# Kernel optimization log

Measured on AMD Instinct MI355X. Metric: run time of the kernel, lower is better.

Reference implementation:

```python
import jax, jax.numpy as jnp
import numpy as np

MAX_VAL = 255.0
C1 = (0.01 * MAX_VAL) ** 2
C2 = (0.03 * MAX_VAL) ** 2


def _gauss_window(ws, sigma, channel=3):
    x = np.arange(ws, dtype=np.float64)
    g = np.exp(-((x - ws // 2) ** 2) / (2.0 * sigma ** 2))
    g = g / g.sum()
    w2 = np.outer(g, g).astype(np.float32)  # [ws, ws]
    w = np.broadcast_to(w2, (channel, 1, ws, ws)).copy()  # depthwise OIHW
    return jnp.asarray(w)


def _dwconv(x, w, pad):
    # depthwise conv2d, NCHW, groups == channels
    return jax.lax.conv_general_dilated(
        x, w, window_strides=(1, 1), padding=[(pad, pad), (pad, pad)],
        dimension_numbers=("NCHW", "OIHW", "NCHW"),
        feature_group_count=x.shape[1])


def _ssim_pair(img1, img2):
    _, c, h, w = img1.shape
    ws = min(h, w, 11)
    sigma = 1.5 * ws / 11.0
    win = _gauss_window(ws, sigma, c)
    pad = ws // 2
    mu1 = _dwconv(img1, win, pad)
    mu2 = _dwconv(img2, win, pad)
    mu1_sq, mu2_sq, mu1_mu2 = mu1 * mu1, mu2 * mu2, mu1 * mu2
    sigma1_sq = _dwconv(img1 * img1, win, pad) - mu1_sq
    sigma2_sq = _dwconv(img2 * img2, win, pad) - mu2_sq
    sigma12 = _dwconv(img1 * img2, win, pad) - mu1_mu2
    V1 = 2.0 * sigma12 + C2
    V2 = sigma1_sq + sigma2_sq + C2
    ssim_map = (2.0 * mu1_mu2 + C1) * V1 / ((mu1_sq + mu2_sq + C1) * V2)
    mcs_map = V1 / V2
    return ssim_map.mean(), mcs_map.mean()


def _avg_pool2(x):
    B, C, H, W = x.shape
    return x.reshape(B, C, H // 2, 2, W // 2, 2).mean(axis=(3, 5))


def _ms_ssim(img1, img2, levels=5):
    weight = jnp.array([0.0448, 0.2856, 0.3001, 0.2363, 0.1333], jnp.float32)
    msssim, mcs = [], []
    for _ in range(levels):
        s, m = _ssim_pair(img1, img2)
        msssim.append(s)
        mcs.append(m)
        img1 = _avg_pool2(img1)
        img2 = _avg_pool2(img2)
    msssim = jnp.stack(msssim)
    mcs = jnp.stack(mcs)
    value = jnp.prod(mcs[: levels - 1] ** weight[: levels - 1]) * msssim[levels - 1] ** weight[levels - 1]
    return 1.0 - value


def _l1_oss(img1, img2):
    _, c, h, w = img1.shape
    ws = min(h, w, 7)
    sigma = 1.1 * ws / 7.0
    win = _gauss_window(ws, sigma, c)
    return _dwconv(jnp.abs(img1 - img2), win, ws // 2).mean()


def _clr_loss(img1, img3):
    _, c, h, w = img1.shape
    ws = min(h, w, 29)
    sigma = ws / 6.0
    win = _gauss_window(ws, sigma, c)
    pad = ws // 2
    mu1 = _dwconv(img1, win, pad)
    mu3 = _dwconv(img3, win, pad)
    cw = [-0.000519, 0.07633, -0.173433, 1.435936, -1.894404, 1.556091]
    # Horner evaluation of cw[5]*x^5 + ... + cw[1]*x + cw[0]
    mu1 = ((((cw[5] * mu1 + cw[4]) * mu1 + cw[3]) * mu1 + cw[2]) * mu1 + cw[1]) * mu1 + cw[0]
    wgray = jnp.array([0.299, 0.587, 0.144], jnp.float32).reshape(1, 3, 1, 1)
    mug1 = (mu1 * wgray).sum(axis=1, keepdims=True)  # 1x1 conv over channels
    mug3 = (mu3 * wgray).sum(axis=1, keepdims=True)
    me1 = mug1.mean(axis=(2, 3), keepdims=True)
    me3 = mug3.mean(axis=(2, 3), keepdims=True)
    sc = me1 / me3
    return jnp.abs(mu1 - mu3 * sc).mean()


def setup_inputs() -> dict:
    key = jax.random.key(0)
    k1, k2, k3 = jax.random.split(key, 3)
    shape = (16, 3, 512, 512)
    return {
        "img1": jax.random.uniform(k1, shape, dtype=jnp.float32),
        "img2": jax.random.uniform(k2, shape, dtype=jnp.float32),
        "img3": jax.random.uniform(k3, shape, dtype=jnp.float32),
    }


def reference(img1, img2, img3):
    l1v = _l1_oss(img1, img2)
    clrv = _clr_loss(img1, img3)
    ssimv = _ms_ssim(img1, img2)
    return 0.4 * ssimv + 0.4 * l1v + 0.2 * clrv
```

## Files before the change

### kernel.cpp

```cpp
#include <hip/hip_runtime.h>
#include <hip/hip_fp16.h>
#include <cmath>

typedef float f2 __attribute__((ext_vector_type(2)));

struct GW7  { float g[7];  };
struct GW11 { float g[11]; };
struct GW29 { float g[29]; };

static void make_gauss(int ws, double sigma, float* out) {
    double t[32]; double s = 0.0;
    int c = ws / 2;
    for (int i = 0; i < ws; ++i) { double d = i - c; t[i] = exp(-(d * d) / (2.0 * sigma * sigma)); s += t[i]; }
    for (int i = 0; i < ws; ++i) out[i] = (float)(t[i] / s);
}

#define ACC_SLOTS 44
#define ACC_BYTES (ACC_SLOTS * 64 * sizeof(double))

__device__ __forceinline__ float poly5(float x) {
    float r = fmaf(1.556091f, x, -1.894404f);
    r = fmaf(r, x, 1.435936f);
    r = fmaf(r, x, -0.173433f);
    r = fmaf(r, x, 0.07633f);
    r = fmaf(r, x, -0.000519f);
    return r;
}

__device__ __forceinline__ float border7(int p, const GW7& gw) {
    if (p >= 3 && p <= 508) return 1.f;
    float r = 0.f;
    #pragma unroll
    for (int k = 0; k < 7; ++k) { int q = p + 3 - k; if (q >= 0 && q < 512) r += gw.g[k]; }
    return r;
}

template<bool INTER>
__global__ __launch_bounds__(256) void ssim_kernel(
    const float* __restrict__ Aim, const float* __restrict__ Bim, const f2* __restrict__ AB,
    int H, int tpp, int tilesX, GW11 gw, GW7 g7, double* __restrict__ acc, int level,
    f2* __restrict__ pooled, int Ho)
{
    constexpr int TILE = 32, IN = 42, SP2 = 46, RP2 = 34;
    __shared__ f2 lds[2 * IN * RP2];
    __shared__ float red[12];
    f2* s    = lds;
    f2* r_mu = lds;
    f2* r_sq = lds + IN * RP2;

    const int tid = threadIdx.x;
    const int bid = blockIdx.x;
    const int plane = bid / tpp;
    const int t = bid - plane * tpp;
    const int ty = t / tilesX, tx = t - ty * tilesX;
    const size_t base = (size_t)plane * H * H;
    const int oy = ty * TILE - 5, ox = tx * TILE - 5;

    for (int i = tid; i < IN * IN; i += 256) {
        int y = i / IN, x = i - y * IN;
        int gy = oy + y, gx = ox + x;
        bool ok = (gy >= 0) && (gy < H) && (gx >= 0) && (gx < H);
        size_t o = base + (size_t)gy * H + gx;
        f2 v = {0.f, 0.f};
        if (ok) {
            if (INTER) v = AB[o];
            else { v.x = Aim[o]; v.y = Bim[o]; }
        }
        s[y * SP2 + x] = v;
    }
    __syncthreads();

    f2 v[18];
    const int ry = tid >> 2, rx0 = (tid & 3) * 8;
    if (tid < IN * 4) {
        #pragma unroll
        for (int l = 0; l < 18; ++l) v[l] = s[ry * SP2 + rx0 + l];
    }
    if (pooled) {
        int py = tid >> 4, px = tid & 15;
        int a = (5 + 2 * py) * SP2 + 5 + 2 * px;
        f2 u = s[a] + s[a + 1] + s[a + SP2] + s[a + SP2 + 1];
        pooled[(size_t)plane * Ho * Ho + (size_t)(ty * 16 + py) * Ho + (tx * 16 + px)] = 0.25f * u;
    }
    float l1p = 0.f;
    if (level == 0) {
        #pragma unroll
        for (int jj = 0; jj < 4; ++jj) {
            int p = jj * 256 + tid;
            int py = p >> 5, px = p & 31;
            f2 u = s[(5 + py) * SP2 + 5 + px];
            float w = border7(ty * 32 + py, g7) * border7(tx * 32 + px, g7);
            l1p += w * fabsf(u.x - u.y);
        }
    }
    __syncthreads();

    if (tid < IN * 4) {
        #pragma unroll
        for (int j = 0; j < 8; ++j) {
            f2 a = {0.f, 0.f};
            #pragma unroll
            for (int k = 0; k < 11; ++k) a = gw.g[k] * v[j + k] + a;
            r_mu[ry * RP2 + rx0 + j] = a;
        }
        #pragma unroll
        for (int l = 0; l < 18; ++l) {
            f2 w;
            w.x = fmaf(v[l].x, v[l].x, v[l].y * v[l].y);
            w.y = v[l].x * v[l].y;
            v[l] = w;
        }
        #pragma unroll
        for (int j = 0; j < 8; ++j) {
            f2 a = {0.f, 0.f};
            #pragma unroll
            for (int k = 0; k < 11; ++k) a = gw.g[k] * v[j + k] + a;
            r_sq[ry * RP2 + rx0 + j] = a;
        }
    }
    __syncthreads();

    const int y0 = (tid >> 5) * 4, x = tid & 31;
    float lss = 0.f, lmc = 0.f;
    {
        f2 mu[4], q[4];
        {
            f2 u[14];
            #pragma unroll
            for (int l = 0; l < 14; ++l) u[l] = r_mu[(y0 + l) * RP2 + x];
            #pragma unroll
            for (int j = 0; j < 4; ++j) {
                f2 a = {0.f, 0.f};
                #pragma unroll
                for (int k = 0; k < 11; ++k) a = gw.g[k] * u[j + k] + a;
                mu[j] = a;
            }
        }
        {
            f2 u[14];
            #pragma unroll
            for (int l = 0; l < 14; ++l) u[l] = r_sq[(y0 + l) * RP2 + x];
            #pragma unroll
            for (int j = 0; j < 4; ++j) {
                f2 a = {0.f, 0.f};
                #pragma unroll
                for (int k = 0; k < 11; ++k) a = gw.g[k] * u[j + k] + a;
                q[j] = a;
            }
        }
        #pragma unroll
        for (int j = 0; j < 4; ++j) {
            float m1 = mu[j].x, m2 = mu[j].y;
            float P = m1 * m2;
            float S = fmaf(m1, m1, m2 * m2);
            float V1 = 2.f * (q[j].y - P) + 58.5225f;
            float V2 = (q[j].x - S) + 58.5225f;
            float num = (2.f * P + 6.5025f) * V1;
            float SC = S + 6.5025f;
            float inv = __builtin_amdgcn_rcpf(SC * V2);
            lss = fmaf(num, inv, lss);
            lmc = fmaf(V1 * SC, inv, lmc);
        }
    }
    #pragma unroll
    for (int o = 32; o > 0; o >>= 1) {
        lss += __shfl_down(lss, o); lmc += __shfl_down(lmc, o); l1p += __shfl_down(l1p, o);
    }
    if ((tid & 63) == 0) {
        int g = tid >> 6;
        red[g * 3] = lss; red[g * 3 + 1] = lmc; red[g * 3 + 2] = l1p;
    }
    __syncthreads();
    if (tid == 0) {
        float a = red[0] + red[3] + red[6] + red[9];
        float m = red[1] + red[4] + red[7] + red[10];
        int stripe = bid & 63;
        atomicAdd(&acc[(0 + level) * 64 + stripe], (double)a);
        atomicAdd(&acc[(5 + level) * 64 + stripe], (double)m);
        if (level == 0) {
            float l1 = red[2] + red[5] + red[8] + red[11];
            atomicAdd(&acc[10 * 64 + stripe], (double)l1);
        }
    }
}

template<int MODE>
__global__ __launch_bounds__(256) void clr_conv(
    const float* __restrict__ img1, const float* __restrict__ img3,
    __half2* __restrict__ pbuf, GW29 gw, double* __restrict__ acc)
{
    constexpr int IN = 60, SP2 = 62, RP2 = 34;
    __shared__ f2 lds[IN * SP2];
    __shared__ float red[8];
    __shared__ float sc_sh;
    f2* s = lds;
    f2* r = lds;

    const int tid = threadIdx.x, bid = blockIdx.x;
    const int plane = bid >> 8, t = bid & 255;
    const int ty = t >> 4, tx = t & 15;
    const int b = plane / 3, c = plane - b * 3;
    const float wg = (c == 0) ? 0.299f : (c == 1 ? 0.587f : 0.144f);
    const size_t base = (size_t)plane * (512 * 512);
    const int oy = ty * 32 - 14, ox = tx * 32 - 14;

    if (MODE == 2 && tid < 64) {
        double m1 = acc[(12 + b) * 64 + tid];
        double m3 = acc[(28 + b) * 64 + tid];
        #pragma unroll
        for (int o = 32; o > 0; o >>= 1) { m1 += __shfl_down(m1, o); m3 += __shfl_down(m3, o); }
        if (tid == 0) sc_sh = (float)(m1 / m3);
    }

    for (int i = tid; i < IN * IN; i += 256) {
        int y = i / IN, x = i - y * IN;
        int gy = oy + y, gx = ox + x;
        bool ok = (gy >= 0) && (gy < 512) && (gx >= 0) && (gx < 512);
        size_t o = base + (size_t)gy * 512 + gx;
        f2 v = {0.f, 0.f};
        if (ok) { v.x = img1[o]; v.y = img3[o]; }
        s[y * SP2 + x] = v;
    }
    __syncthreads();

    f2 v[36];
    const int ry = tid >> 2, rx0 = (tid & 3) * 8;
    if (tid < IN * 4) {
        #pragma unroll
        for (int l = 0; l < 36; ++l) v[l] = s[ry * SP2 + rx0 + l];
    }
    __syncthreads();
    if (tid < IN * 4) {
        #pragma unroll
        for (int j = 0; j < 8; ++j) {
            f2 a = {0.f, 0.f};
            #pragma unroll
            for (int k = 0; k < 29; ++k) a = gw.g[k] * v[j + k] + a;
            r[ry * RP2 + rx0 + j] = a;
        }
    }
    __syncthreads();

    const int y0 = (tid >> 5) * 4, x = tid & 31;
    f2 mu[4];
    {
        f2 u[32];
        #pragma unroll
        for (int l = 0; l < 32; ++l) u[l] = r[(y0 + l) * RP2 + x];
        #pragma unroll
        for (int j = 0; j < 4; ++j) {
            f2 a = {0.f, 0.f};
            #pragma unroll
            for (int k = 0; k < 29; ++k) a = gw.g[k] * u[j + k] + a;
            mu[j] = a;
        }
    }
    float p1 = 0.f, p3 = 0.f;
    #pragma unroll
    for (int j = 0; j < 4; ++j) {
        float p = poly5(mu[j].x);
        if (MODE == 2) {
            p1 += fabsf(p - mu[j].y * sc_sh);
        } else {
            p1 += p; p3 += mu[j].y;
            if (MODE == 0)
                pbuf[base + (size_t)(ty * 32 + y0 + j) * 512 + (tx * 32 + x)] =
                    __floats2half2_rn(p, mu[j].y);
        }
    }
    if (MODE != 2) { p1 *= wg; p3 *= wg; }
    #pragma unroll
    for (int o = 32; o > 0; o >>= 1) { p1 += __shfl_down(p1, o); p3 += __shfl_down(p3, o); }
    if ((tid & 63) == 0) { red[(tid >> 6) * 2] = p1; red[(tid >> 6) * 2 + 1] = p3; }
    __syncthreads();
    if (tid == 0) {
        float a1 = red[0] + red[2] + red[4] + red[6];
        int stripe = bid & 63;
        if (MODE == 2) {
            atomicAdd(&acc[11 * 64 + stripe], (double)a1);
        } else {
            float a3 = red[1] + red[3] + red[5] + red[7];
            atomicAdd(&acc[(12 + b) * 64 + stripe], (double)a1);
            atomicAdd(&acc[(28 + b) * 64 + stripe], (double)a3);
        }
    }
}

__global__ __launch_bounds__(256) void clr_fin(
    const __half2* __restrict__ pbuf, double* __restrict__ acc)
{
    __shared__ float red[4];
    __shared__ float sc_sh;
    const int tid = threadIdx.x, bid = blockIdx.x;
    const int b = bid / 192, sub = bid - b * 192;
    if (tid < 64) {
        double m1 = acc[(12 + b) * 64 + tid];
        double m3 = acc[(28 + b) * 64 + tid];
        #pragma unroll
        for (int o = 32; o > 0; o >>= 1) { m1 += __shfl_down(m1, o); m3 += __shfl_down(m3, o); }
        if (tid == 0) sc_sh = (float)(m1 / m3);
    }
    __syncthreads();
    const float sc = sc_sh;
    const size_t bo = (size_t)b * 786432 + (size_t)sub * 4096;
    float s = 0.f;
    #pragma unroll
    for (int it = 0; it < 8; ++it) {
        size_t i = bo + it * 512 + tid * 2;
        float2 a = __half22float2(pbuf[i]);
        float2 c = __half22float2(pbuf[i + 1]);
        s += fabsf(a.x - a.y * sc) + fabsf(c.x - c.y * sc);
    }
    #pragma unroll
    for (int o = 32; o > 0; o >>= 1) s += __shfl_down(s, o);
    if ((tid & 63) == 0) red[tid >> 6] = s;
    __syncthreads();
    if (tid == 0)
        atomicAdd(&acc[11 * 64 + (bid & 63)], (double)(red[0] + red[1] + red[2] + red[3]));
}

__global__ void finalize_kernel(const double* __restrict__ acc, float* __restrict__ out)
{
    __shared__ double sums[ACC_SLOTS];
    int t = threadIdx.x;
    if (t < ACC_SLOTS) {
        double s = 0.0;
        for (int i = 0; i < 64; ++i) s += acc[t * 64 + i];
        sums[t] = s;
    }
    __syncthreads();
    if (t == 0) {
        const double w[5] = {0.0448, 0.2856, 0.3001, 0.2363, 0.1333};
        double value = 1.0;
        for (int l = 0; l < 5; ++l) {
            double dim = (double)(512 >> l);
            double cnt = 48.0 * dim * dim;
            double mval = (l < 4) ? (sums[5 + l] / cnt) : (sums[l] / cnt);
            value *= pow(mval, w[l]);
        }
        double n0 = 48.0 * 512.0 * 512.0;
        double l1v = sums[10] / n0;
        double clrv = sums[11] / n0;
        out[0] = (float)(0.4 * (1.0 - value) + 0.4 * l1v + 0.2 * clrv);
    }
}

extern "C" void kernel_launch(void* const* d_in, const int* in_sizes, int n_in,
                              void* d_out, int out_size, void* d_ws, size_t ws_size,
                              hipStream_t stream)
{
    (void)in_sizes; (void)n_in; (void)out_size;
    const float* img1 = (const float*)d_in[0];
    const float* img2 = (const float*)d_in[1];
    const float* img3 = (const float*)d_in[2];
    float* out = (float*)d_out;
    double* acc = (double*)d_ws;

    GW11 g11; make_gauss(11, 1.5, g11.g);
    GW7  g7;  make_gauss(7, 1.1, g7.g);
    GW29 g29; make_gauss(29, 29.0 / 6.0, g29.g);

    hipMemsetAsync(d_ws, 0, ACC_BYTES, stream);

    f2* pyr = (f2*)((char*)d_ws + 32768);
    size_t offs[4];
    offs[0] = 0;
    offs[1] = offs[0] + (size_t)48 * 256 * 256;
    offs[2] = offs[1] + (size_t)48 * 128 * 128;
    offs[3] = offs[2] + (size_t)48 * 64 * 64;
    const size_t PYRF2 = offs[3] + (size_t)48 * 32 * 32;

    const f2* cur = nullptr;
    int H = 512;
    for (int l = 0; l < 5; ++l) {
        int tilesX = H / 32; int tpp = tilesX * tilesX;
        f2* pooled = (l < 4) ? (pyr + offs[l]) : nullptr;
        int Ho = H / 2;
        if (l == 0)
            ssim_kernel<false><<<48 * tpp, 256, 0, stream>>>(
                img1, img2, nullptr, H, tpp, tilesX, g11, g7, acc, l, pooled, Ho);
        else
            ssim_kernel<true><<<48 * tpp, 256, 0, stream>>>(
                nullptr, nullptr, cur, H, tpp, tilesX, g11, g7, acc, l, pooled, Ho);
        cur = pooled; H = Ho;
    }

    const size_t poff = 32768 + PYRF2 * sizeof(f2);
    const size_t PBYTES = (size_t)48 * 512 * 512 * sizeof(__half2);
    __half2* pbuf = (__half2*)((char*)d_ws + poff);
    if (ws_size >= poff + PBYTES) {
        clr_conv<0><<<12288, 256, 0, stream>>>(img1, img3, pbuf, g29, acc);
        clr_fin<<<3072, 256, 0, stream>>>(pbuf, acc);
    } else {
        clr_conv<1><<<12288, 256, 0, stream>>>(img1, img3, pbuf, g29, acc);
        clr_conv<2><<<12288, 256, 0, stream>>>(img1, img3, pbuf, g29, acc);
    }

    finalize_kernel<<<1, 64, 0, stream>>>(acc, out);
}
```

Before: 236.3 us.

## Stream convolution taps to cut register pressure and split LDS buffers

The separable Gaussian passes in the SSIM and colour kernels now accumulate outputs while streaming input values, instead of holding whole input windows in registers. This lowers register use and may raise occupancy. The SSIM kernel gives the source tile and the two row-pass results their own LDS buffers with odd strides, which removes one barrier and aims to reduce bank conflicts but uses more shared memory. The colour kernel loads its 60-row halo in two 30-row chunks with 240 threads doing the horizontal pass, trading an extra barrier pair for a smaller staging buffer.

```diff
diff --git a/kernel.cpp b/kernel.cpp
--- a/kernel.cpp
+++ b/kernel.cpp
@@ -35,18 +35,19 @@
     return r;
 }
 
+#define SSP 47
+#define SRP 33
 template<bool INTER>
 __global__ __launch_bounds__(256) void ssim_kernel(
     const float* __restrict__ Aim, const float* __restrict__ Bim, const f2* __restrict__ AB,
     int H, int tpp, int tilesX, GW11 gw, GW7 g7, double* __restrict__ acc, int level,
     f2* __restrict__ pooled, int Ho)
 {
-    constexpr int TILE = 32, IN = 42, SP2 = 46, RP2 = 34;
-    __shared__ f2 lds[2 * IN * RP2];
+    constexpr int TILE = 32, IN = 42;
+    __shared__ f2 s[IN * SSP];
+    __shared__ f2 r_mu[IN * SRP];
+    __shared__ f2 r_sq[IN * SRP];
     __shared__ float red[12];
-    f2* s    = lds;
-    f2* r_mu = lds;
-    f2* r_sq = lds + IN * RP2;
 
     const int tid = threadIdx.x;
     const int bid = blockIdx.x;
@@ -66,20 +67,40 @@
             if (INTER) v = AB[o];
             else { v.x = Aim[o]; v.y = Bim[o]; }
         }
-        s[y * SP2 + x] = v;
-    }
-    __syncthreads();
-
-    f2 v[18];
-    const int ry = tid >> 2, rx0 = (tid & 3) * 8;
+        s[y * SSP + x] = v;
+    }
+    __syncthreads();
+
     if (tid < IN * 4) {
-        #pragma unroll
-        for (int l = 0; l < 18; ++l) v[l] = s[ry * SP2 + rx0 + l];
+        const int ry = tid >> 2, rx0 = (tid & 3) * 8;
+        f2 mu[8], q[8];
+        #pragma unroll
+        for (int j = 0; j < 8; ++j) { mu[j] = (f2){0.f, 0.f}; q[j] = (f2){0.f, 0.f}; }
+        #pragma unroll
+        for (int l = 0; l < 18; ++l) {
+            f2 val = s[ry * SSP + rx0 + l];
+            f2 sq;
+            sq.x = fmaf(val.x, val.x, val.y * val.y);
+            sq.y = val.x * val.y;
+            #pragma unroll
+            for (int j = 0; j < 8; ++j) {
+                if (l - j >= 0 && l - j < 11) {
+                    float g = gw.g[l - j];
+                    mu[j] = g * val + mu[j];
+                    q[j]  = g * sq  + q[j];
+                }
+            }
+        }
+        #pragma unroll
+        for (int j = 0; j < 8; ++j) {
+            r_mu[ry * SRP + rx0 + j] = mu[j];
+            r_sq[ry * SRP + rx0 + j] = q[j];
+        }
     }
     if (pooled) {
         int py = tid >> 4, px = tid & 15;
-        int a = (5 + 2 * py) * SP2 + 5 + 2 * px;
-        f2 u = s[a] + s[a + 1] + s[a + SP2] + s[a + SP2 + 1];
+        int a = (5 + 2 * py) * SSP + 5 + 2 * px;
+        f2 u = s[a] + s[a + 1] + s[a + SSP] + s[a + SSP + 1];
         pooled[(size_t)plane * Ho * Ho + (size_t)(ty * 16 + py) * Ho + (tx * 16 + px)] = 0.25f * u;
     }
     float l1p = 0.f;
@@ -88,34 +109,9 @@
         for (int jj = 0; jj < 4; ++jj) {
             int p = jj * 256 + tid;
             int py = p >> 5, px = p & 31;
-            f2 u = s[(5 + py) * SP2 + 5 + px];
+            f2 u = s[(5 + py) * SSP + 5 + px];
             float w = border7(ty * 32 + py, g7) * border7(tx * 32 + px, g7);
             l1p += w * fabsf(u.x - u.y);
-        }
-    }
-    __syncthreads();
-
-    if (tid < IN * 4) {
-        #pragma unroll
-        for (int j = 0; j < 8; ++j) {
-            f2 a = {0.f, 0.f};
-            #pragma unroll
-            for (int k = 0; k < 11; ++k) a = gw.g[k] * v[j + k] + a;
-            r_mu[ry * RP2 + rx0 + j] = a;
-        }
-        #pragma unroll
-        for (int l = 0; l < 18; ++l) {
-            f2 w;
-            w.x = fmaf(v[l].x, v[l].x, v[l].y * v[l].y);
-            w.y = v[l].x * v[l].y;
-            v[l] = w;
-        }
-        #pragma unroll
-        for (int j = 0; j < 8; ++j) {
-            f2 a = {0.f, 0.f};
-            #pragma unroll
-            for (int k = 0; k < 11; ++k) a = gw.g[k] * v[j + k] + a;
-            r_sq[ry * RP2 + rx0 + j] = a;
         }
     }
     __syncthreads();
@@ -124,29 +120,23 @@
     float lss = 0.f, lmc = 0.f;
     {
         f2 mu[4], q[4];
-        {
-            f2 u[14];
-            #pragma unroll
-            for (int l = 0; l < 14; ++l) u[l] = r_mu[(y0 + l) * RP2 + x];
-            #pragma unroll
-            for (int j = 0; j < 4; ++j) {
-                f2 a = {0.f, 0.f};
-                #pragma unroll
-                for (int k = 0; k < 11; ++k) a = gw.g[k] * u[j + k] + a;
-                mu[j] = a;
-            }
-        }
-        {
-            f2 u[14];
-            #pragma unroll
-            for (int l = 0; l < 14; ++l) u[l] = r_sq[(y0 + l) * RP2 + x];
-            #pragma unroll
-            for (int j = 0; j < 4; ++j) {
-                f2 a = {0.f, 0.f};
-                #pragma unroll
-                for (int k = 0; k < 11; ++k) a = gw.g[k] * u[j + k] + a;
-                q[j] = a;
-            }
+        #pragma unroll
+        for (int j = 0; j < 4; ++j) mu[j] = (f2){0.f, 0.f};
+        #pragma unroll
+        for (int l = 0; l < 14; ++l) {
+            f2 val = r_mu[(y0 + l) * SRP + x];
+            #pragma unroll
+            for (int j = 0; j < 4; ++j)
+                if (l - j >= 0 && l - j < 11) mu[j] = gw.g[l - j] * val + mu[j];
+        }
+        #pragma unroll
+        for (int j = 0; j < 4; ++j) q[j] = (f2){0.f, 0.f};
+        #pragma unroll
+        for (int l = 0; l < 14; ++l) {
+            f2 val = r_sq[(y0 + l) * SRP + x];
+            #pragma unroll
+            for (int j = 0; j < 4; ++j)
+                if (l - j >= 0 && l - j < 11) q[j] = gw.g[l - j] * val + q[j];
         }
         #pragma unroll
         for (int j = 0; j < 4; ++j) {
@@ -184,17 +174,17 @@
     }
 }
 
+#define CSP 63
+#define CRP 33
 template<int MODE>
 __global__ __launch_bounds__(256) void clr_conv(
     const float* __restrict__ img1, const float* __restrict__ img3,
     __half2* __restrict__ pbuf, GW29 gw, double* __restrict__ acc)
 {
-    constexpr int IN = 60, SP2 = 62, RP2 = 34;
-    __shared__ f2 lds[IN * SP2];
+    __shared__ f2 sc[30 * CSP];
+    __shared__ f2 r[60 * CRP];
     __shared__ float red[8];
     __shared__ float sc_sh;
-    f2* s = lds;
-    f2* r = lds;
 
     const int tid = threadIdx.x, bid = blockIdx.x;
     const int plane = bid >> 8, t = bid & 255;
@@ -212,48 +202,46 @@
         if (tid == 0) sc_sh = (float)(m1 / m3);
     }
 
-    for (int i = tid; i < IN * IN; i += 256) {
-        int y = i / IN, x = i - y * IN;
-        int gy = oy + y, gx = ox + x;
-        bool ok = (gy >= 0) && (gy < 512) && (gx >= 0) && (gx < 512);
-        size_t o = base + (size_t)gy * 512 + gx;
-        f2 v = {0.f, 0.f};
-        if (ok) { v.x = img1[o]; v.y = img3[o]; }
-        s[y * SP2 + x] = v;
-    }
-    __syncthreads();
-
-    f2 v[36];
-    const int ry = tid >> 2, rx0 = (tid & 3) * 8;
-    if (tid < IN * 4) {
-        #pragma unroll
-        for (int l = 0; l < 36; ++l) v[l] = s[ry * SP2 + rx0 + l];
-    }
-    __syncthreads();
-    if (tid < IN * 4) {
-        #pragma unroll
-        for (int j = 0; j < 8; ++j) {
-            f2 a = {0.f, 0.f};
-            #pragma unroll
-            for (int k = 0; k < 29; ++k) a = gw.g[k] * v[j + k] + a;
-            r[ry * RP2 + rx0 + j] = a;
-        }
-    }
-    __syncthreads();
+    #pragma unroll
+    for (int ck = 0; ck < 2; ++ck) {
+        for (int i = tid; i < 30 * 60; i += 256) {
+            int y = i / 60, x = i - y * 60;
+            int gy = oy + ck * 30 + y, gx = ox + x;
+            bool ok = (gy >= 0) && (gy < 512) && (gx >= 0) && (gx < 512);
+            size_t o = base + (size_t)gy * 512 + gx;
+            f2 v = {0.f, 0.f};
+            if (ok) { v.x = img1[o]; v.y = img3[o]; }
+            sc[y * CSP + x] = v;
+        }
+        __syncthreads();
+        if (tid < 240) {
+            int yl = tid >> 3, x0 = (tid & 7) * 4;
+            f2 a[4];
+            #pragma unroll
+            for (int j = 0; j < 4; ++j) a[j] = (f2){0.f, 0.f};
+            #pragma unroll
+            for (int l = 0; l < 32; ++l) {
+                f2 val = sc[yl * CSP + x0 + l];
+                #pragma unroll
+                for (int j = 0; j < 4; ++j)
+                    if (l - j >= 0 && l - j < 29) a[j] = gw.g[l - j] * val + a[j];
+            }
+            #pragma unroll
+            for (int j = 0; j < 4; ++j) r[(ck * 30 + yl) * CRP + x0 + j] = a[j];
+        }
+        __syncthreads();
+    }
 
     const int y0 = (tid >> 5) * 4, x = tid & 31;
     f2 mu[4];
-    {
-        f2 u[32];
-        #pragma unroll
-        for (int l = 0; l < 32; ++l) u[l] = r[(y0 + l) * RP2 + x];
-        #pragma unroll
-        for (int j = 0; j < 4; ++j) {
-            f2 a = {0.f, 0.f};
-            #pragma unroll
-            for (int k = 0; k < 29; ++k) a = gw.g[k] * u[j + k] + a;
-            mu[j] = a;
-        }
+    #pragma unroll
+    for (int j = 0; j < 4; ++j) mu[j] = (f2){0.f, 0.f};
+    #pragma unroll
+    for (int l = 0; l < 32; ++l) {
+        f2 val = r[(y0 + l) * CRP + x];
+        #pragma unroll
+        for (int j = 0; j < 4; ++j)
+            if (l - j >= 0 && l - j < 29) mu[j] = gw.g[l - j] * val + mu[j];
     }
     float p1 = 0.f, p3 = 0.f;
     #pragma unroll
```

Result: slower. 263.0 us (+11.3%).

## Load CLR conv rows directly from global with float4 and repad LDS strides

Applied to the files above, without the earlier changes.

The CLR Gaussian conv kernel no longer stages the 60x60 input tile in shared memory. Each thread reads its row segment from global memory with float4 loads into registers and runs the horizontal 29-tap pass there, processing img1 and img3 one after the other. This removes a staging pass and a barrier and shrinks LDS use. Separately, the LDS row strides in both kernels become odd (49 and 33 f2 elements) to reduce bank conflicts. The trade-offs are more register pressure and redundant global reads of the overlapping halo, which the cache has to absorb.

```diff
diff --git a/kernel.cpp b/kernel.cpp
--- a/kernel.cpp
+++ b/kernel.cpp
@@ -35,18 +35,20 @@
     return r;
 }
 
+#define SSP 49
+#define SRP 33
 template<bool INTER>
 __global__ __launch_bounds__(256) void ssim_kernel(
     const float* __restrict__ Aim, const float* __restrict__ Bim, const f2* __restrict__ AB,
     int H, int tpp, int tilesX, GW11 gw, GW7 g7, double* __restrict__ acc, int level,
     f2* __restrict__ pooled, int Ho)
 {
-    constexpr int TILE = 32, IN = 42, SP2 = 46, RP2 = 34;
-    __shared__ f2 lds[2 * IN * RP2];
+    constexpr int TILE = 32, IN = 42;
+    __shared__ f2 lds[2 * IN * SRP];
     __shared__ float red[12];
     f2* s    = lds;
     f2* r_mu = lds;
-    f2* r_sq = lds + IN * RP2;
+    f2* r_sq = lds + IN * SRP;
 
     const int tid = threadIdx.x;
     const int bid = blockIdx.x;
@@ -66,7 +68,7 @@
             if (INTER) v = AB[o];
             else { v.x = Aim[o]; v.y = Bim[o]; }
         }
-        s[y * SP2 + x] = v;
+        s[y * SSP + x] = v;
     }
     __syncthreads();
 
@@ -74,12 +76,12 @@
     const int ry = tid >> 2, rx0 = (tid & 3) * 8;
     if (tid < IN * 4) {
         #pragma unroll
-        for (int l = 0; l < 18; ++l) v[l] = s[ry * SP2 + rx0 + l];
+        for (int l = 0; l < 18; ++l) v[l] = s[ry * SSP + rx0 + l];
     }
     if (pooled) {
         int py = tid >> 4, px = tid & 15;
-        int a = (5 + 2 * py) * SP2 + 5 + 2 * px;
-        f2 u = s[a] + s[a + 1] + s[a + SP2] + s[a + SP2 + 1];
+        int a = (5 + 2 * py) * SSP + 5 + 2 * px;
+        f2 u = s[a] + s[a + 1] + s[a + SSP] + s[a + SSP + 1];
         pooled[(size_t)plane * Ho * Ho + (size_t)(ty * 16 + py) * Ho + (tx * 16 + px)] = 0.25f * u;
     }
     float l1p = 0.f;
@@ -88,7 +90,7 @@
         for (int jj = 0; jj < 4; ++jj) {
             int p = jj * 256 + tid;
             int py = p >> 5, px = p & 31;
-            f2 u = s[(5 + py) * SP2 + 5 + px];
+            f2 u = s[(5 + py) * SSP + 5 + px];
             float w = border7(ty * 32 + py, g7) * border7(tx * 32 + px, g7);
             l1p += w * fabsf(u.x - u.y);
         }
@@ -101,7 +103,7 @@
             f2 a = {0.f, 0.f};
             #pragma unroll
             for (int k = 0; k < 11; ++k) a = gw.g[k] * v[j + k] + a;
-            r_mu[ry * RP2 + rx0 + j] = a;
+            r_mu[ry * SRP + rx0 + j] = a;
         }
         #pragma unroll
         for (int l = 0; l < 18; ++l) {
@@ -115,7 +117,7 @@
             f2 a = {0.f, 0.f};
             #pragma unroll
             for (int k = 0; k < 11; ++k) a = gw.g[k] * v[j + k] + a;
-            r_sq[ry * RP2 + rx0 + j] = a;
+            r_sq[ry * SRP + rx0 + j] = a;
         }
     }
     __syncthreads();
@@ -127,7 +129,7 @@
         {
             f2 u[14];
             #pragma unroll
-            for (int l = 0; l < 14; ++l) u[l] = r_mu[(y0 + l) * RP2 + x];
+            for (int l = 0; l < 14; ++l) u[l] = r_mu[(y0 + l) * SRP + x];
             #pragma unroll
             for (int j = 0; j < 4; ++j) {
                 f2 a = {0.f, 0.f};
@@ -139,7 +141,7 @@
         {
             f2 u[14];
             #pragma unroll
-            for (int l = 0; l < 14; ++l) u[l] = r_sq[(y0 + l) * RP2 + x];
+            for (int l = 0; l < 14; ++l) u[l] = r_sq[(y0 + l) * SRP + x];
             #pragma unroll
             for (int j = 0; j < 4; ++j) {
                 f2 a = {0.f, 0.f};
@@ -184,17 +186,15 @@
     }
 }
 
+#define CRP 33
 template<int MODE>
 __global__ __launch_bounds__(256) void clr_conv(
     const float* __restrict__ img1, const float* __restrict__ img3,
     __half2* __restrict__ pbuf, GW29 gw, double* __restrict__ acc)
 {
-    constexpr int IN = 60, SP2 = 62, RP2 = 34;
-    __shared__ f2 lds[IN * SP2];
+    __shared__ f2 r[60 * CRP];
     __shared__ float red[8];
     __shared__ float sc_sh;
-    f2* s = lds;
-    f2* r = lds;
 
     const int tid = threadIdx.x, bid = blockIdx.x;
     const int plane = bid >> 8, t = bid & 255;
@@ -202,7 +202,6 @@
     const int b = plane / 3, c = plane - b * 3;
     const float wg = (c == 0) ? 0.299f : (c == 1 ? 0.587f : 0.144f);
     const size_t base = (size_t)plane * (512 * 512);
-    const int oy = ty * 32 - 14, ox = tx * 32 - 14;
 
     if (MODE == 2 && tid < 64) {
         double m1 = acc[(12 + b) * 64 + tid];
@@ -212,31 +211,42 @@
         if (tid == 0) sc_sh = (float)(m1 / m3);
     }
 
-    for (int i = tid; i < IN * IN; i += 256) {
-        int y = i / IN, x = i - y * IN;
-        int gy = oy + y, gx = ox + x;
-        bool ok = (gy >= 0) && (gy < 512) && (gx >= 0) && (gx < 512);
-        size_t o = base + (size_t)gy * 512 + gx;
-        f2 v = {0.f, 0.f};
-        if (ok) { v.x = img1[o]; v.y = img3[o]; }
-        s[y * SP2 + x] = v;
-    }
-    __syncthreads();
-
-    f2 v[36];
-    const int ry = tid >> 2, rx0 = (tid & 3) * 8;
-    if (tid < IN * 4) {
-        #pragma unroll
-        for (int l = 0; l < 36; ++l) v[l] = s[ry * SP2 + rx0 + l];
-    }
-    __syncthreads();
-    if (tid < IN * 4) {
+    if (tid < 240) {
+        const int ry = tid >> 2, xq = tid & 3;
+        const int gy = ty * 32 - 14 + ry;
+        const bool vr = (gy >= 0) && (gy < 512);
+        const int c0 = tx * 8 + xq * 2 - 4;
+        const float4* row1 = (const float4*)(img1 + base + (size_t)(vr ? gy : 0) * 512);
+        const float4* row3 = (const float4*)(img3 + base + (size_t)(vr ? gy : 0) * 512);
+        float w[40];
+        float o1[8];
+        #pragma unroll
+        for (int k = 0; k < 10; ++k) {
+            int cc = c0 + k;
+            float4 f = {0.f, 0.f, 0.f, 0.f};
+            if (vr && cc >= 0 && cc < 128) f = row1[cc];
+            w[4 * k] = f.x; w[4 * k + 1] = f.y; w[4 * k + 2] = f.z; w[4 * k + 3] = f.w;
+        }
         #pragma unroll
         for (int j = 0; j < 8; ++j) {
-            f2 a = {0.f, 0.f};
-            #pragma unroll
-            for (int k = 0; k < 29; ++k) a = gw.g[k] * v[j + k] + a;
-            r[ry * RP2 + rx0 + j] = a;
+            float a = 0.f;
+            #pragma unroll
+            for (int k = 0; k < 29; ++k) a = fmaf(gw.g[k], w[2 + j + k], a);
+            o1[j] = a;
+        }
+        #pragma unroll
+        for (int k = 0; k < 10; ++k) {
+            int cc = c0 + k;
+            float4 f = {0.f, 0.f, 0.f, 0.f};
+            if (vr && cc >= 0 && cc < 128) f = row3[cc];
+            w[4 * k] = f.x; w[4 * k + 1] = f.y; w[4 * k + 2] = f.z; w[4 * k + 3] = f.w;
+        }
+        #pragma unroll
+        for (int j = 0; j < 8; ++j) {
+            float a = 0.f;
+            #pragma unroll
+            for (int k = 0; k < 29; ++k) a = fmaf(gw.g[k], w[2 + j + k], a);
+            r[ry * CRP + xq * 8 + j] = (f2){o1[j], a};
         }
     }
     __syncthreads();
@@ -246,7 +256,7 @@
     {
         f2 u[32];
         #pragma unroll
-        for (int l = 0; l < 32; ++l) u[l] = r[(y0 + l) * RP2 + x];
+        for (int l = 0; l < 32; ++l) u[l] = r[(y0 + l) * CRP + x];
         #pragma unroll
         for (int j = 0; j < 4; ++j) {
             f2 a = {0.f, 0.f};
```

Result: no change. 237.2 us (+0.4%).
